# Performance work log

Hardware: AMD Instinct MI355X
Metric: run time of the kernel (lower is better)

Reference implementation:

```python
import jax, jax.numpy as jnp
import numpy as np

T = 35            # cfg.VOXEL_POINT_COUNT
D, H, W = 10, 400, 352  # cfg.INPUT_DEPTH/HEIGHT/WIDTH
EPS = 1e-5


def _vfe(x, mask, w, b, gamma, beta):
    # x: [K, T, Cin]; mask: [K, T, 1]
    h = jax.nn.relu(jnp.einsum('ktc,cu->ktu', x, w) + b)        # [K, T, U]
    mean = jnp.mean(h, axis=(0, 1))
    var = jnp.var(h, axis=(0, 1))
    h = (h - mean) * jax.lax.rsqrt(var + EPS) * gamma + beta    # batch-stat BN
    agg = jnp.max(h, axis=1, keepdims=True)                     # [K, 1, U]
    cat = jnp.concatenate([h, jnp.broadcast_to(agg, h.shape)], axis=-1)  # [K, T, 2U]
    return cat * mask


def setup_inputs() -> dict:
    key = jax.random.key(0)
    ks = jax.random.split(key, 12)
    K = 40000
    feature = jax.random.normal(ks[0], (K, T, 7), dtype=jnp.float32)
    # zero out ~half the points so the nonzero mask is meaningful
    keep = jax.random.bernoulli(ks[1], 0.5, (K, T, 1)).astype(jnp.float32)
    feature = feature * keep
    bidx = jax.random.randint(ks[2], (K, 1), 0, 2)
    didx = jax.random.randint(ks[3], (K, 1), 0, D)
    hidx = jax.random.randint(ks[4], (K, 1), 0, H)
    widx = jax.random.randint(ks[5], (K, 1), 0, W)
    coordinate = jnp.concatenate([bidx, didx, hidx, widx], axis=1).astype(jnp.int32)
    s = 0.1
    return {
        'feature': feature,
        'w1': jax.random.normal(ks[6], (7, 16), dtype=jnp.float32) * s,
        'b1': jnp.zeros((16,), dtype=jnp.float32),
        'gamma1': jnp.ones((16,), dtype=jnp.float32),
        'beta1': jnp.zeros((16,), dtype=jnp.float32),
        'w2': jax.random.normal(ks[7], (32, 32), dtype=jnp.float32) * s,
        'b2': jnp.zeros((32,), dtype=jnp.float32),
        'gamma2': jnp.ones((32,), dtype=jnp.float32),
        'beta2': jnp.zeros((32,), dtype=jnp.float32),
        'coordinate': coordinate,
        'batch_size': 2,
    }


def reference(feature, w1, b1, gamma1, beta1, w2, b2, gamma2, beta2, coordinate, batch_size):
    # mask: voxel point is valid if any channel nonzero (max over channels != 0)
    mask = (jnp.max(feature, axis=2, keepdims=True) != 0).astype(feature.dtype)  # [K, T, 1]
    x = _vfe(feature, mask, w1, b1, gamma1, beta1)   # [K, T, 32]
    x = _vfe(x, mask, w2, b2, gamma2, beta2)         # [K, T, 64]
    voxelwise = jnp.max(x, axis=1)                   # [K, 64]
    out = jnp.zeros((batch_size, D, H, W, 64), dtype=voxelwise.dtype)
    out = out.at[coordinate[:, 0], coordinate[:, 1], coordinate[:, 2], coordinate[:, 3]].add(voxelwise)
    return out
```

## Files before the change

kernel.cpp:

```cpp
#include <hip/hip_runtime.h>
#include <math.h>

#define TT 35
#define DD 10
#define HD 400
#define WD 352
#define CIN 7
#define U1 16
#define U2 32
#define EPSV 1e-5f

#define WS_A1 0
#define WS_B1 16
#define WS_A2 32
#define WS_B2 64
#define WS_SUM1 256
#define WS_SSQ1 768
#define WS_SUM2 1280
#define WS_SSQ2 3328
#define NC1 32
#define NC2 64
#define WS_ZERO_FLOATS 5376

__global__ __launch_bounds__(256) void k_stats1(
    const float* __restrict__ feat, const float* __restrict__ w1,
    const float* __restrict__ b1, float* __restrict__ ws, int P) {
  __shared__ float s_w1[CIN * U1];
  __shared__ float s_b1[U1];
  __shared__ float s_red[4][2 * U1];

  int tid = threadIdx.x;
  if (tid < CIN * U1) s_w1[tid] = w1[tid];
  if (tid < U1) s_b1[tid] = b1[tid];
  __syncthreads();

  float sum[U1], ssq[U1];
#pragma unroll
  for (int u = 0; u < U1; ++u) { sum[u] = 0.f; ssq[u] = 0.f; }

  int stride = gridDim.x * blockDim.x;
  for (int p = blockIdx.x * blockDim.x + tid; p < P; p += stride) {
    const float* f = feat + (size_t)p * CIN;
    float x[CIN];
#pragma unroll
    for (int c = 0; c < CIN; ++c) x[c] = f[c];
#pragma unroll
    for (int u = 0; u < U1; ++u) {
      float acc = s_b1[u];
#pragma unroll
      for (int c = 0; c < CIN; ++c) acc += x[c] * s_w1[c * U1 + u];
      float h = fmaxf(acc, 0.f);
      sum[u] += h;
      ssq[u] += h * h;
    }
  }

  int lane = tid & 63, wv = tid >> 6;
#pragma unroll
  for (int u = 0; u < U1; ++u) {
    float s = sum[u], q = ssq[u];
    for (int off = 32; off; off >>= 1) {
      s += __shfl_down(s, off);
      q += __shfl_down(q, off);
    }
    if (lane == 0) { s_red[wv][u] = s; s_red[wv][U1 + u] = q; }
  }
  __syncthreads();
  if (tid < 2 * U1) {
    float tot = s_red[0][tid] + s_red[1][tid] + s_red[2][tid] + s_red[3][tid];
    int copy = blockIdx.x & (NC1 - 1);
    int u = tid & (U1 - 1);
    int base = (tid < U1) ? WS_SUM1 : WS_SSQ1;
    atomicAdd(&ws[base + copy * U1 + u], tot);
  }
}

__global__ void k_fin1(const float* __restrict__ gamma,
                       const float* __restrict__ beta, float* __restrict__ ws,
                       float invN) {
  int u = threadIdx.x;
  float s = 0.f, q = 0.f;
  for (int c = 0; c < NC1; ++c) {
    s += ws[WS_SUM1 + c * U1 + u];
    q += ws[WS_SSQ1 + c * U1 + u];
  }
  float mean = s * invN;
  float var = q * invN - mean * mean;
  float istd = 1.0f / sqrtf(var + EPSV);
  float A = gamma[u] * istd;
  ws[WS_A1 + u] = A;
  ws[WS_B1 + u] = beta[u] - mean * A;
}

__global__ void k_fin2(const float* __restrict__ gamma,
                       const float* __restrict__ beta, float* __restrict__ ws,
                       float invN) {
  int u = threadIdx.x;
  float s = 0.f, q = 0.f;
  for (int c = 0; c < NC2; ++c) {
    s += ws[WS_SUM2 + c * U2 + u];
    q += ws[WS_SSQ2 + c * U2 + u];
  }
  float mean = s * invN;
  float var = q * invN - mean * mean;
  float istd = 1.0f / sqrtf(var + EPSV);
  float A = gamma[u] * istd;
  ws[WS_A2 + u] = A;
  ws[WS_B2 + u] = beta[u] - mean * A;
}

template <bool FINAL>
__global__ __launch_bounds__(256) void k_vfe(
    const float* __restrict__ feat, const float* __restrict__ w1,
    const float* __restrict__ b1, const float* __restrict__ w2,
    const float* __restrict__ b2, const int* __restrict__ coord,
    float* __restrict__ ws, float* __restrict__ out, int K) {
  __shared__ float s_w1t[U1][9];
  __shared__ __align__(16) float s_w2t[U2 * U2];
  __shared__ float s_b1[U1], s_A1[U1], s_B1[U1];
  __shared__ float s_b2[U2], s_A2[U2], s_B2[U2];
  __shared__ float s_feat[4][TT * 9];
  __shared__ __align__(16) float s_cat[4][TT][U2];
  __shared__ float s_agg[4][U1];
  __shared__ float s_red[4][2 * U2];
  __shared__ __align__(16) float s_h2[FINAL ? 4 : 1][TT][U2];

  int tid = threadIdx.x;
  int lane = tid & 63, wv = tid >> 6;
  int v = blockIdx.x * 4 + wv;
  bool active = (v < K);

  if (tid < CIN * U1) {
    int u = tid / CIN, c = tid % CIN;
    s_w1t[u][c] = w1[c * U1 + u];
  }
  for (int i = tid; i < U2 * U2; i += 256) {
    int u = i >> 5, c = i & 31;
    s_w2t[i] = w2[c * U2 + u];
  }
  if (tid < U1) {
    s_b1[tid] = b1[tid];
    s_A1[tid] = ws[WS_A1 + tid];
    s_B1[tid] = ws[WS_B1 + tid];
  }
  if (tid < U2) {
    s_b2[tid] = b2[tid];
    s_A2[tid] = ws[WS_A2 + tid];
    s_B2[tid] = ws[WS_B2 + tid];
  }
  __syncthreads();

  if (active) {
    const float* fv = feat + (size_t)v * TT * CIN;
    for (int i = lane; i < TT * CIN; i += 64) {
      int t = i / CIN, c = i % CIN;
      s_feat[wv][t * 9 + c] = fv[i];
    }
  }
  __syncthreads();
  if (active && lane < TT) {
    float m = s_feat[wv][lane * 9 + 0];
#pragma unroll
    for (int c = 1; c < CIN; ++c) m = fmaxf(m, s_feat[wv][lane * 9 + c]);
    s_feat[wv][lane * 9 + 7] = (m != 0.f) ? 1.f : 0.f;
  }
  __syncthreads();

  if (active) {
    for (int i = lane; i < TT * U1; i += 64) {
      int t = i >> 4, u = i & 15;
      float acc = s_b1[u];
#pragma unroll
      for (int c = 0; c < CIN; ++c) acc += s_feat[wv][t * 9 + c] * s_w1t[u][c];
      float h = fmaxf(acc, 0.f);
      s_cat[wv][t][u] = s_A1[u] * h + s_B1[u];
    }
  }
  __syncthreads();
  if (active && lane < U1) {
    float m = s_cat[wv][0][lane];
    for (int t = 1; t < TT; ++t) m = fmaxf(m, s_cat[wv][t][lane]);
    s_agg[wv][lane] = m;
  }
  __syncthreads();
  if (active) {
    for (int i = lane; i < TT * U1; i += 64) {
      int t = i >> 4, u = i & 15;
      float mk = s_feat[wv][t * 9 + 7];
      s_cat[wv][t][u] *= mk;
      s_cat[wv][t][U1 + u] = s_agg[wv][u] * mk;
    }
  }
  __syncthreads();

  int u = lane & 31;
  int th = lane >> 5;
  float rw2[U2];
#pragma unroll
  for (int c4 = 0; c4 < 8; ++c4) {
    float4 v4 = *(const float4*)&s_w2t[u * U2 + 4 * c4];
    rw2[4 * c4 + 0] = v4.x;
    rw2[4 * c4 + 1] = v4.y;
    rw2[4 * c4 + 2] = v4.z;
    rw2[4 * c4 + 3] = v4.w;
  }
  float b2u = s_b2[u], A2u = s_A2[u], B2u = s_B2[u];
  float sum2 = 0.f, ssq2 = 0.f;
  if (active) {
    for (int t = th; t < TT; t += 2) {
      float acc = b2u;
      const float4* cr = (const float4*)&s_cat[wv][t][0];
#pragma unroll
      for (int c4 = 0; c4 < 8; ++c4) {
        float4 v4 = cr[c4];
        acc += v4.x * rw2[4 * c4] + v4.y * rw2[4 * c4 + 1] +
               v4.z * rw2[4 * c4 + 2] + v4.w * rw2[4 * c4 + 3];
      }
      float h = fmaxf(acc, 0.f);
      if (FINAL) {
        s_h2[wv][t][u] = A2u * h + B2u;
      } else {
        sum2 += h;
        ssq2 += h * h;
      }
    }
  }

  if (!FINAL) {
    float o1 = __shfl_down(sum2, 32);
    float o2 = __shfl_down(ssq2, 32);
    if (lane < 32) {
      s_red[wv][lane] = sum2 + o1;
      s_red[wv][U2 + lane] = ssq2 + o2;
    }
    __syncthreads();
    if (tid < 2 * U2) {
      float tot = s_red[0][tid] + s_red[1][tid] + s_red[2][tid] + s_red[3][tid];
      int copy = blockIdx.x & (NC2 - 1);
      int ch = tid & (U2 - 1);
      int base = (tid < U2) ? WS_SUM2 : WS_SSQ2;
      atomicAdd(&ws[base + copy * U2 + ch], tot);
    }
  } else {
    __syncthreads();
    float aggv = 0.f;
    if (active && lane < U2) {
      float m = s_h2[wv][0][lane];
      for (int t = 1; t < TT; ++t) m = fmaxf(m, s_h2[wv][t][lane]);
      aggv = m;
    }
    float aggb = __shfl(aggv, lane & 31);
    if (active) {
      int c = lane;
      float vox = -INFINITY;
      for (int t = 0; t < TT; ++t) {
        float mk = s_feat[wv][t * 9 + 7];
        float val = (c < U2) ? s_h2[wv][t][c] : aggb;
        vox = fmaxf(vox, val * mk);
      }
      const int4 cd = *(const int4*)&coord[4 * v];
      long base =
          ((((long)cd.x * DD + cd.y) * HD + cd.z) * WD + cd.w) * 64;
      atomicAdd(&out[base + c], vox);
    }
  }
}

extern "C" void kernel_launch(void* const* d_in, const int* in_sizes, int n_in,
                              void* d_out, int out_size, void* d_ws,
                              size_t ws_size, hipStream_t stream) {
  const float* feat = (const float*)d_in[0];
  const float* w1 = (const float*)d_in[1];
  const float* b1 = (const float*)d_in[2];
  const float* g1 = (const float*)d_in[3];
  const float* be1 = (const float*)d_in[4];
  const float* w2 = (const float*)d_in[5];
  const float* b2 = (const float*)d_in[6];
  const float* g2 = (const float*)d_in[7];
  const float* be2 = (const float*)d_in[8];
  const int* coord = (const int*)d_in[9];
  float* out = (float*)d_out;
  float* ws = (float*)d_ws;

  int K = in_sizes[0] / (TT * CIN);
  int P = K * TT;
  float invN = 1.0f / (float)P;

  (void)hipMemsetAsync(d_out, 0, (size_t)out_size * sizeof(float), stream);
  (void)hipMemsetAsync(d_ws, 0, WS_ZERO_FLOATS * sizeof(float), stream);

  k_stats1<<<512, 256, 0, stream>>>(feat, w1, b1, ws, P);
  k_fin1<<<1, U1, 0, stream>>>(g1, be1, ws, invN);

  int vb = (K + 3) / 4;
  k_vfe<false><<<vb, 256, 0, stream>>>(feat, w1, b1, w2, b2, nullptr, ws,
                                       nullptr, K);
  k_fin2<<<1, U2, 0, stream>>>(g2, be2, ws, invN);
  k_vfe<true><<<vb, 256, 0, stream>>>(feat, w1, b1, w2, b2, coord, ws, out, K);
}
```

Baseline: 1.023 ms.

## Store layer-2 activations to workspace and fuse output zeroing into stats pass

The layer-2 stats kernel now writes the pre-BN activations and the point mask to workspace. A lightweight final kernel then reads them back to apply BN, compute the max-aggregate and the voxel max, instead of recomputing both VFE layers from the features. Zeroing the large output tensor moves from a memset into a grid-stride loop inside the stats kernel. This trades recompute for about 180 MB of extra global writes and reads. The stored path only runs if the workspace is large enough, otherwise the old recompute path is used.

```diff
diff --git a/kernel.cpp b/kernel.cpp
--- a/kernel.cpp
+++ b/kernel.cpp
@@ -21,6 +21,7 @@
 #define NC1 32
 #define NC2 64
 #define WS_ZERO_FLOATS 5376
+#define WS_H2_OFF 8192
 
 __global__ __launch_bounds__(256) void k_stats1(
     const float* __restrict__ feat, const float* __restrict__ w1,
@@ -109,8 +110,170 @@
   ws[WS_B2 + u] = beta[u] - mean * A;
 }
 
-template <bool FINAL>
-__global__ __launch_bounds__(256) void k_vfe(
+template <bool STORE>
+__global__ __launch_bounds__(256) void k_vfe2(
+    const float* __restrict__ feat, const float* __restrict__ w1,
+    const float* __restrict__ b1, const float* __restrict__ w2,
+    const float* __restrict__ b2, float* __restrict__ ws,
+    float* __restrict__ h2g, float* __restrict__ maskg,
+    float4* __restrict__ out4, long n4, int K) {
+  __shared__ float s_w1t[U1][9];
+  __shared__ __align__(16) float s_w2t[U2 * U2];
+  __shared__ float s_b1[U1], s_A1[U1], s_B1[U1];
+  __shared__ float s_b2[U2];
+  __shared__ float s_feat[4][TT * 9];
+  __shared__ __align__(16) float s_cat[4][TT][U2];
+  __shared__ float s_agg[4][U1];
+  __shared__ float s_red[4][2 * U2];
+
+  int tid = threadIdx.x;
+  int lane = tid & 63, wv = tid >> 6;
+  int v = blockIdx.x * 4 + wv;
+  bool active = (v < K);
+
+  if (tid < CIN * U1) {
+    int u = tid / CIN, c = tid % CIN;
+    s_w1t[u][c] = w1[c * U1 + u];
+  }
+  for (int i = tid; i < U2 * U2; i += 256) {
+    int u = i >> 5, c = i & 31;
+    s_w2t[i] = w2[c * U2 + u];
+  }
+  if (tid < U1) {
+    s_b1[tid] = b1[tid];
+    s_A1[tid] = ws[WS_A1 + tid];
+    s_B1[tid] = ws[WS_B1 + tid];
+  }
+  if (tid < U2) s_b2[tid] = b2[tid];
+  __syncthreads();
+
+  if (active) {
+    const float* fv = feat + (size_t)v * TT * CIN;
+    for (int i = lane; i < TT * CIN; i += 64) {
+      int t = i / CIN, c = i % CIN;
+      s_feat[wv][t * 9 + c] = fv[i];
+    }
+  }
+  __syncthreads();
+  if (active && lane < TT) {
+    float m = s_feat[wv][lane * 9 + 0];
+#pragma unroll
+    for (int c = 1; c < CIN; ++c) m = fmaxf(m, s_feat[wv][lane * 9 + c]);
+    float mk = (m != 0.f) ? 1.f : 0.f;
+    s_feat[wv][lane * 9 + 7] = mk;
+    if (STORE) maskg[(size_t)v * TT + lane] = mk;
+  }
+  __syncthreads();
+
+  if (active) {
+    for (int i = lane; i < TT * U1; i += 64) {
+      int t = i >> 4, u = i & 15;
+      float acc = s_b1[u];
+#pragma unroll
+      for (int c = 0; c < CIN; ++c) acc += s_feat[wv][t * 9 + c] * s_w1t[u][c];
+      float h = fmaxf(acc, 0.f);
+      s_cat[wv][t][u] = s_A1[u] * h + s_B1[u];
+    }
+  }
+  __syncthreads();
+  if (active && lane < U1) {
+    float m = s_cat[wv][0][lane];
+    for (int t = 1; t < TT; ++t) m = fmaxf(m, s_cat[wv][t][lane]);
+    s_agg[wv][lane] = m;
+  }
+  __syncthreads();
+  if (active) {
+    for (int i = lane; i < TT * U1; i += 64) {
+      int t = i >> 4, u = i & 15;
+      float mk = s_feat[wv][t * 9 + 7];
+      s_cat[wv][t][u] *= mk;
+      s_cat[wv][t][U1 + u] = s_agg[wv][u] * mk;
+    }
+  }
+  __syncthreads();
+
+  int u = lane & 31;
+  int th = lane >> 5;
+  float rw2[U2];
+#pragma unroll
+  for (int c4 = 0; c4 < 8; ++c4) {
+    float4 v4 = *(const float4*)&s_w2t[u * U2 + 4 * c4];
+    rw2[4 * c4 + 0] = v4.x;
+    rw2[4 * c4 + 1] = v4.y;
+    rw2[4 * c4 + 2] = v4.z;
+    rw2[4 * c4 + 3] = v4.w;
+  }
+  float b2u = s_b2[u];
+  float sum2 = 0.f, ssq2 = 0.f;
+  if (active) {
+    for (int t = th; t < TT; t += 2) {
+      float acc = b2u;
+      const float4* cr = (const float4*)&s_cat[wv][t][0];
+#pragma unroll
+      for (int c4 = 0; c4 < 8; ++c4) {
+        float4 v4 = cr[c4];
+        acc += v4.x * rw2[4 * c4] + v4.y * rw2[4 * c4 + 1] +
+               v4.z * rw2[4 * c4 + 2] + v4.w * rw2[4 * c4 + 3];
+      }
+      float h = fmaxf(acc, 0.f);
+      if (STORE) h2g[((size_t)v * TT + t) * U2 + u] = h;
+      sum2 += h;
+      ssq2 += h * h;
+    }
+  }
+
+  float o1 = __shfl_down(sum2, 32);
+  float o2 = __shfl_down(ssq2, 32);
+  if (lane < 32) {
+    s_red[wv][lane] = sum2 + o1;
+    s_red[wv][U2 + lane] = ssq2 + o2;
+  }
+  __syncthreads();
+  if (tid < 2 * U2) {
+    float tot = s_red[0][tid] + s_red[1][tid] + s_red[2][tid] + s_red[3][tid];
+    int copy = blockIdx.x & (NC2 - 1);
+    int ch = tid & (U2 - 1);
+    int base = (tid < U2) ? WS_SUM2 : WS_SSQ2;
+    atomicAdd(&ws[base + copy * U2 + ch], tot);
+  }
+
+  long gtid = (long)blockIdx.x * 256 + tid;
+  long gstride = (long)gridDim.x * 256;
+  float4 z = make_float4(0.f, 0.f, 0.f, 0.f);
+  for (long i = gtid; i < n4; i += gstride) out4[i] = z;
+}
+
+__global__ __launch_bounds__(256) void k_final(
+    const float* __restrict__ h2g, const float* __restrict__ maskg,
+    const float* __restrict__ ws, const int* __restrict__ coord,
+    float* __restrict__ out, int K) {
+  int tid = threadIdx.x;
+  int lane = tid & 63, wv = tid >> 6;
+  int v = blockIdx.x * 4 + wv;
+  if (v >= K) return;
+  int ch = lane & 31;
+  float A2 = ws[WS_A2 + ch], B2 = ws[WS_B2 + ch];
+  const float* hrow = h2g + (size_t)v * TT * U2 + ch;
+  const float* mrow = maskg + (size_t)v * TT;
+  float agg = -INFINITY, vox = -INFINITY;
+  bool any1 = false, any0 = false;
+#pragma unroll 5
+  for (int t = 0; t < TT; ++t) {
+    float h = hrow[(size_t)t * U2];
+    float mk = mrow[t];
+    float hn = A2 * h + B2;
+    agg = fmaxf(agg, hn);
+    vox = fmaxf(vox, hn * mk);
+    any1 |= (mk != 0.f);
+    any0 |= (mk == 0.f);
+  }
+  if (lane >= 32) vox = any1 ? (any0 ? fmaxf(agg, 0.f) : agg) : 0.f;
+  const int4 cd = *(const int4*)&coord[4 * v];
+  long base = ((((long)cd.x * DD + cd.y) * HD + cd.z) * WD + cd.w) * 64;
+  atomicAdd(&out[base + lane], vox);
+}
+
+__global__ __launch_bounds__(256) void k_vfe_final_recompute(
     const float* __restrict__ feat, const float* __restrict__ w1,
     const float* __restrict__ b1, const float* __restrict__ w2,
     const float* __restrict__ b2, const int* __restrict__ coord,
@@ -122,8 +285,7 @@
   __shared__ float s_feat[4][TT * 9];
   __shared__ __align__(16) float s_cat[4][TT][U2];
   __shared__ float s_agg[4][U1];
-  __shared__ float s_red[4][2 * U2];
-  __shared__ __align__(16) float s_h2[FINAL ? 4 : 1][TT][U2];
+  __shared__ __align__(16) float s_h2[4][TT][U2];
 
   int tid = threadIdx.x;
   int lane = tid & 63, wv = tid >> 6;
@@ -205,7 +367,6 @@
     rw2[4 * c4 + 3] = v4.w;
   }
   float b2u = s_b2[u], A2u = s_A2[u], B2u = s_B2[u];
-  float sum2 = 0.f, ssq2 = 0.f;
   if (active) {
     for (int t = th; t < TT; t += 2) {
       float acc = b2u;
@@ -217,52 +378,29 @@
                v4.z * rw2[4 * c4 + 2] + v4.w * rw2[4 * c4 + 3];
       }
       float h = fmaxf(acc, 0.f);
-      if (FINAL) {
-        s_h2[wv][t][u] = A2u * h + B2u;
-      } else {
-        sum2 += h;
-        ssq2 += h * h;
-      }
-    }
-  }
-
-  if (!FINAL) {
-    float o1 = __shfl_down(sum2, 32);
-    float o2 = __shfl_down(ssq2, 32);
-    if (lane < 32) {
-      s_red[wv][lane] = sum2 + o1;
-      s_red[wv][U2 + lane] = ssq2 + o2;
-    }
-    __syncthreads();
-    if (tid < 2 * U2) {
-      float tot = s_red[0][tid] + s_red[1][tid] + s_red[2][tid] + s_red[3][tid];
-      int copy = blockIdx.x & (NC2 - 1);
-      int ch = tid & (U2 - 1);
-      int base = (tid < U2) ? WS_SUM2 : WS_SSQ2;
-      atomicAdd(&ws[base + copy * U2 + ch], tot);
-    }
-  } else {
-    __syncthreads();
-    float aggv = 0.f;
-    if (active && lane < U2) {
-      float m = s_h2[wv][0][lane];
-      for (int t = 1; t < TT; ++t) m = fmaxf(m, s_h2[wv][t][lane]);
-      aggv = m;
-    }
-    float aggb = __shfl(aggv, lane & 31);
-    if (active) {
-      int c = lane;
-      float vox = -INFINITY;
-      for (int t = 0; t < TT; ++t) {
-        float mk = s_feat[wv][t * 9 + 7];
-        float val = (c < U2) ? s_h2[wv][t][c] : aggb;
-        vox = fmaxf(vox, val * mk);
-      }
-      const int4 cd = *(const int4*)&coord[4 * v];
-      long base =
-          ((((long)cd.x * DD + cd.y) * HD + cd.z) * WD + cd.w) * 64;
-      atomicAdd(&out[base + c], vox);
-    }
+      s_h2[wv][t][u] = A2u * h + B2u;
+    }
+  }
+  __syncthreads();
+
+  float aggv = 0.f;
+  if (active && lane < U2) {
+    float m = s_h2[wv][0][lane];
+    for (int t = 1; t < TT; ++t) m = fmaxf(m, s_h2[wv][t][lane]);
+    aggv = m;
+  }
+  float aggb = __shfl(aggv, lane & 31);
+  if (active) {
+    int c = lane;
+    float vox = -INFINITY;
+    for (int t = 0; t < TT; ++t) {
+      float mk = s_feat[wv][t * 9 + 7];
+      float val = (c < U2) ? s_h2[wv][t][c] : aggb;
+      vox = fmaxf(vox, val * mk);
+    }
+    const int4 cd = *(const int4*)&coord[4 * v];
+    long base = ((((long)cd.x * DD + cd.y) * HD + cd.z) * WD + cd.w) * 64;
+    atomicAdd(&out[base + c], vox);
   }
 }
 
@@ -285,16 +423,30 @@
   int K = in_sizes[0] / (TT * CIN);
   int P = K * TT;
   float invN = 1.0f / (float)P;
-
-  (void)hipMemsetAsync(d_out, 0, (size_t)out_size * sizeof(float), stream);
+  long n4 = (long)out_size / 4;
+
+  size_t need_bytes =
+      ((size_t)WS_H2_OFF + (size_t)K * TT * U2 + (size_t)K * TT) * 4;
+  bool store = ws_size >= need_bytes;
+  float* h2g = ws + WS_H2_OFF;
+  float* maskg = h2g + (size_t)K * TT * U2;
+
   (void)hipMemsetAsync(d_ws, 0, WS_ZERO_FLOATS * sizeof(float), stream);
 
   k_stats1<<<512, 256, 0, stream>>>(feat, w1, b1, ws, P);
   k_fin1<<<1, U1, 0, stream>>>(g1, be1, ws, invN);
 
   int vb = (K + 3) / 4;
-  k_vfe<false><<<vb, 256, 0, stream>>>(feat, w1, b1, w2, b2, nullptr, ws,
-                                       nullptr, K);
-  k_fin2<<<1, U2, 0, stream>>>(g2, be2, ws, invN);
-  k_vfe<true><<<vb, 256, 0, stream>>>(feat, w1, b1, w2, b2, coord, ws, out, K);
-}
+  if (store) {
+    k_vfe2<true><<<vb, 256, 0, stream>>>(feat, w1, b1, w2, b2, ws, h2g, maskg,
+                                         (float4*)out, n4, K);
+    k_fin2<<<1, U2, 0, stream>>>(g2, be2, ws, invN);
+    k_final<<<vb, 256, 0, stream>>>(h2g, maskg, ws, coord, out, K);
+  } else {
+    k_vfe2<false><<<vb, 256, 0, stream>>>(feat, w1, b1, w2, b2, ws, nullptr,
+                                          nullptr, (float4*)out, n4, K);
+    k_fin2<<<1, U2, 0, stream>>>(g2, be2, ws, invN);
+    k_vfe_final_recompute<<<vb, 256, 0, stream>>>(feat, w1, b1, w2, b2, coord,
+                                                  ws, out, K);
+  }
+}
```

Result: faster. 915.5 us (-10.5%).
